# Kernel tuning notes

Hardware: AMD Instinct MI355X
Metric: run time of the kernel (lower is better)

## Reference

```python
import jax, jax.numpy as jnp
import numpy as np

N = 1_000_000   # detections
FDIM = 64       # embedding dim
C = 128         # number of clusters (track ids in [0, C))
DELTA_VAR = 0.5
DELTA_DIST = 3.0


def setup_inputs() -> dict:
    key = jax.random.key(0)
    k1, k2 = jax.random.split(key)
    features = jax.random.normal(k1, (N, FDIM), dtype=jnp.float32)
    labels = jax.random.randint(k2, (N, 2), 0, C, dtype=jnp.int32)  # [fr, track_id], all ids >= 0
    return {"features": features, "labels": labels}


def reference(features, labels):
    # All track ids are >= 0 by construction, so the tp_ids filter is a no-op
    # and the dynamic unique-cluster loop becomes a fixed-C segment reduce.
    ids = labels[:, 1]
    ones = jnp.ones((features.shape[0],), dtype=features.dtype)
    counts = jax.ops.segment_sum(ones, ids, num_segments=C)            # (C,)
    sums = jax.ops.segment_sum(features, ids, num_segments=C)         # (C, F)
    means = sums / counts[:, None]                                     # per-cluster mean

    # variance term: per-point distance to its cluster mean, hinged at delta_var
    d = jnp.linalg.norm(features - means[ids], axis=1)                 # (N,)
    per_pt = jnp.square(jax.nn.relu(d - DELTA_VAR))
    per_cluster = jax.ops.segment_sum(per_pt, ids, num_segments=C) / counts
    var_loss = jnp.sum(per_cluster) / C

    # pairwise cluster-distance term over i != j, hinged at delta_dist
    diff = means[:, None, :] - means[None, :, :]                       # (C, C, F)
    sq = jnp.sum(diff * diff, axis=-1)                                 # (C, C)
    eye = jnp.eye(C, dtype=bool)
    pd = jnp.sqrt(jnp.where(eye, 1.0, sq))                             # safe sqrt on diagonal
    dl = jnp.where(eye, 0.0, jnp.square(jax.nn.relu(DELTA_DIST - pd)))
    dist_loss = jnp.sum(dl) / (C * (C - 1))

    return var_loss + dist_loss
```

## Files before the change

kernel.cpp:

```cpp
#include <hip/hip_runtime.h>

#define NPTS 1000000
#define FDIM 64
#define CNUM 128
#define PSTRIDE 8320
#define NB1 1024
#define NB3 1024

typedef _Float16 half8 __attribute__((ext_vector_type(8)));
typedef float f32x4 __attribute__((ext_vector_type(4)));

__global__ __launch_bounds__(256, 4) void k1_partials(
    const float* __restrict__ feats, const int* __restrict__ labels,
    float* __restrict__ partials, int nblocks)
{
    __shared__ float lds[FDIM * 132];
    __shared__ float cnt[CNUM];
    const int tid = threadIdx.x;
    if (tid < CNUM) cnt[tid] = 0.f;
    __syncthreads();

    const int lane = tid & 63;
    const int n15 = lane & 15;
    const int kb = (lane >> 4) * 8;
    const int rowb = (lane >> 4) * 4;
    const int w = tid >> 6;
    const int fh = w & 1;
    const int fbase = fh * 32;
    const int nstreams = nblocks * 2;
    const int ts = ((blockIdx.x << 2) + w) >> 1;

    f32x4 acc[8][2];
    #pragma unroll
    for (int ct = 0; ct < 8; ++ct)
        #pragma unroll
        for (int nt = 0; nt < 2; ++nt)
            acc[ct][nt] = (f32x4){0.f, 0.f, 0.f, 0.f};

    const int ntiles = NPTS / 32;
    for (int t = ts; t < ntiles; t += nstreams) {
        const int p0 = t * 32;
        const float* fp = feats + (size_t)(p0 + kb) * FDIM + fbase + n15;
        const int* lp = labels + 2 * (p0 + kb) + 1;
        int vlab[8];
        #pragma unroll
        for (int i = 0; i < 8; ++i) vlab[i] = lp[2 * i];

        half8 B[2];
        #pragma unroll
        for (int nt = 0; nt < 2; ++nt) {
            #pragma unroll
            for (int i = 0; i < 8; ++i)
                B[nt][i] = (_Float16)fp[i * FDIM + nt * 16];
        }
        if (fh == 0 && lane < 32) {
            const int myl = labels[2 * (p0 + lane) + 1];
            atomicAdd(&cnt[myl], 1.0f);
        }
        #pragma unroll
        for (int ct = 0; ct < 8; ++ct) {
            const int cmine = ct * 16 + n15;
            union { unsigned u[4]; half8 h; } ua;
            #pragma unroll
            for (int j = 0; j < 4; ++j)
                ua.u[j] = ((vlab[2 * j] == cmine) ? 0x3C00u : 0u)
                        | ((vlab[2 * j + 1] == cmine) ? 0x3C000000u : 0u);
            #pragma unroll
            for (int nt = 0; nt < 2; ++nt)
                acc[ct][nt] = __builtin_amdgcn_mfma_f32_16x16x32_f16(
                    ua.h, B[nt], acc[ct][nt], 0, 0, 0);
        }
    }
    __syncthreads();

    for (int r = 0; r < 2; ++r) {
        if ((w >> 1) == r) {
            #pragma unroll
            for (int ct = 0; ct < 8; ++ct)
                #pragma unroll
                for (int nt = 0; nt < 2; ++nt) {
                    float* a = &lds[(fbase + nt * 16 + n15) * 132 + ct * 16 + rowb];
                    if (r == 0) *(f32x4*)a = acc[ct][nt];
                    else        *(f32x4*)a = *(f32x4*)a + acc[ct][nt];
                }
        }
        __syncthreads();
    }

    float* dst = partials + (size_t)blockIdx.x * PSTRIDE;
    for (int i4 = tid; i4 < 2048; i4 += 256) {
        const int f = i4 >> 5, c0 = (i4 & 31) * 4;
        ((float4*)dst)[i4] = *(float4*)&lds[f * 132 + c0];
    }
    if (tid < CNUM) dst[8192 + tid] = cnt[tid];
}

__global__ __launch_bounds__(256) void k2_reduce(
    const float* __restrict__ partials, int nblocks, float* __restrict__ red,
    float* __restrict__ ppsum, float* __restrict__ dsum, int* __restrict__ counter)
{
    const int tid = threadIdx.x;
    const int tsub = tid & 31, grp = tid >> 5;
    const int t0 = blockIdx.x * 32;
    float s = 0.f;
    #pragma unroll 8
    for (int b = grp; b < nblocks; b += 8)
        s += partials[(size_t)b * PSTRIDE + t0 + tsub];
    __shared__ float lred[8][33];
    lred[grp][tsub] = s;
    __syncthreads();
    if (tid < 32) {
        float tot = 0.f;
        #pragma unroll
        for (int q = 0; q < 8; ++q) tot += lred[q][tid];
        const int t = t0 + tid;
        if (t < 8192) red[(t & 127) * FDIM + (t >> 7)] = tot;
        else red[t] = tot;
    }
    if (blockIdx.x == 0) {
        if (tid >= 128) ppsum[tid - 128] = 0.f;
        if (tid == 64) dsum[0] = 0.f;
        if (tid == 65) counter[0] = 0;
    }
}

__global__ __launch_bounds__(256, 4) void k3_var(
    const float4* __restrict__ feats4, const int* __restrict__ labels,
    const float* __restrict__ red, float* __restrict__ ppsum, int nblocks)
{
    __shared__ float4 mu4[CNUM * 16];
    __shared__ float lpp[CNUM];
    const int tid = threadIdx.x;
    for (int i = tid; i < 2048; i += 256) {
        float4 sv = ((const float4*)red)[i];
        float ci = 1.0f / red[8192 + (i >> 4)];
        mu4[i] = make_float4(sv.x * ci, sv.y * ci, sv.z * ci, sv.w * ci);
    }
    if (tid < CNUM) lpp[tid] = 0.f;
    __syncthreads();

    const int lane = tid & 63;
    const int k = lane & 15, g = lane >> 4;
    const int nwaves = nblocks * 4;
    const int wid = ((blockIdx.x << 8) + tid) >> 6;
    const int ntiles = NPTS / 16;

    int b = wid;
    float4 v[4]; int cc = 0;
    if (b < ntiles) {
        const float4* fp = feats4 + (size_t)b * 256 + lane;
        #pragma unroll
        for (int s = 0; s < 4; ++s) v[s] = fp[s * 64];
        cc = labels[2 * (b * 16 + k) + 1];
    }
    while (b < ntiles) {
        const int bn = b + nwaves;
        float4 vn[4]; int ccn = 0;
        if (bn < ntiles) {
            const float4* fp = feats4 + (size_t)bn * 256 + lane;
            #pragma unroll
            for (int s = 0; s < 4; ++s) vn[s] = fp[s * 64];
            ccn = labels[2 * (bn * 16 + k) + 1];
        }
        #pragma unroll
        for (int s = 0; s < 4; ++s) {
            const int c = __shfl(cc, 4 * s + g);
            float4 m = mu4[c * 16 + k];
            float dx = v[s].x - m.x, dy = v[s].y - m.y,
                  dz = v[s].z - m.z, dw = v[s].w - m.w;
            float sq = dx * dx + dy * dy + dz * dz + dw * dw;
            sq += __shfl_xor(sq, 1); sq += __shfl_xor(sq, 2);
            sq += __shfl_xor(sq, 4); sq += __shfl_xor(sq, 8);
            if (k == 0) {
                const float t = sqrtf(sq) - 0.5f;
                if (t > 0.f) atomicAdd(&lpp[c], t * t);
            }
        }
        b = bn;
        #pragma unroll
        for (int s = 0; s < 4; ++s) v[s] = vn[s];
        cc = ccn;
    }
    __syncthreads();
    if (tid < CNUM) atomicAdd(&ppsum[tid], lpp[tid]);
}

__global__ __launch_bounds__(128) void k45_dist_final(
    const float* __restrict__ red, const float* __restrict__ ppsum,
    float* __restrict__ dsum, int* __restrict__ counter, float* __restrict__ out)
{
    __shared__ float4 mu4[CNUM * 17];
    __shared__ int lastflag;
    __shared__ float sv[2];
    const int tid = threadIdx.x;
    for (int i = tid; i < 2048; i += 128) {
        float4 s4 = ((const float4*)red)[i];
        float ci = 1.0f / red[8192 + (i >> 4)];
        mu4[(i >> 4) * 17 + (i & 15)] =
            make_float4(s4.x * ci, s4.y * ci, s4.z * ci, s4.w * ci);
    }
    __syncthreads();
    const int i = blockIdx.x, j = tid;
    float sq = 0.f;
    #pragma unroll
    for (int q = 0; q < 16; ++q) {
        float4 a = mu4[i * 17 + q], b = mu4[j * 17 + q];
        float dx = a.x - b.x, dy = a.y - b.y, dz = a.z - b.z, dw = a.w - b.w;
        sq += dx * dx + dy * dy + dz * dz + dw * dw;
    }
    float dl = 0.f;
    if (j != i) {
        const float r = 3.0f - sqrtf(sq);
        if (r > 0.f) dl = r * r;
    }
    #pragma unroll
    for (int m = 1; m < 64; m <<= 1) dl += __shfl_xor(dl, m);
    if ((tid & 63) == 0) atomicAdd(dsum, dl);
    __threadfence();
    __syncthreads();
    if (tid == 0) lastflag = (atomicAdd(counter, 1) == (int)gridDim.x - 1);
    __syncthreads();
    if (lastflag) {
        float v = ppsum[tid] / red[8192 + tid];
        #pragma unroll
        for (int m = 1; m < 64; m <<= 1) v += __shfl_xor(v, m);
        if ((tid & 63) == 0) sv[tid >> 6] = v;
    }
    __syncthreads();
    if (lastflag && tid == 0) {
        const float dtot = atomicAdd(dsum, 0.0f);
        out[0] = (sv[0] + sv[1]) / (float)CNUM
               + dtot / (float)(CNUM * (CNUM - 1));
    }
}

extern "C" void kernel_launch(void* const* d_in, const int* in_sizes, int n_in,
                              void* d_out, int out_size, void* d_ws, size_t ws_size,
                              hipStream_t stream) {
    (void)in_sizes; (void)n_in; (void)out_size;
    const float* feats   = (const float*)d_in[0];
    const float4* feats4 = (const float4*)d_in[0];
    const int* labels    = (const int*)d_in[1];
    float* ws            = (float*)d_ws;
    float* out           = (float*)d_out;

    int nb1 = NB1;
    {
        size_t avail = ws_size / sizeof(float);
        size_t fixed = PSTRIDE + 128 + 2;
        if (avail > fixed) {
            size_t cap = (avail - fixed) / PSTRIDE;
            if ((size_t)nb1 > cap) nb1 = (int)cap;
        } else nb1 = 1;
        if (nb1 < 1) nb1 = 1;
    }
    float* partials = ws;
    float* red      = ws + (size_t)nb1 * PSTRIDE;
    float* ppsum    = red + PSTRIDE;
    float* dsum     = ppsum + 128;
    int*   counter  = (int*)(dsum + 1);

    k1_partials<<<nb1, 256, 0, stream>>>(feats, labels, partials, nb1);
    k2_reduce<<<PSTRIDE / 32, 256, 0, stream>>>(partials, nb1, red, ppsum, dsum, counter);
    k3_var<<<NB3, 256, 0, stream>>>(feats4, labels, red, ppsum, NB3);
    k45_dist_final<<<CNUM, 128, 0, stream>>>(red, ppsum, dsum, counter, out);
}
```

Before: 132.9 us.

## Split k1 feature dims across four waves, prefetch next tile, drop LDS reduction

Each of the four waves in a k1 block now owns a distinct 16-feature slice of one shared 32-point tile, instead of pairs of waves handling 32 features on separate tile streams. The next tile's features and labels are register-prefetched while the current tile's MFMAs run. Accumulators are written straight to global memory in cluster-major order, which removes the LDS cross-wave reduction and the transposition in k2. The grid grows to 1280 blocks with an occupancy hint of 5, and k2 is reshaped to 16 columns by 16 block-groups, at the cost of more partial buffers to reduce and uncoalesced scattered stores from k1.

```diff
diff --git a/kernel.cpp b/kernel.cpp
--- a/kernel.cpp
+++ b/kernel.cpp
@@ -4,17 +4,16 @@
 #define FDIM 64
 #define CNUM 128
 #define PSTRIDE 8320
-#define NB1 1024
+#define NB1 1280
 #define NB3 1024
 
 typedef _Float16 half8 __attribute__((ext_vector_type(8)));
 typedef float f32x4 __attribute__((ext_vector_type(4)));
 
-__global__ __launch_bounds__(256, 4) void k1_partials(
+__global__ __launch_bounds__(256, 5) void k1_partials(
     const float* __restrict__ feats, const int* __restrict__ labels,
     float* __restrict__ partials, int nblocks)
 {
-    __shared__ float lds[FDIM * 132];
     __shared__ float cnt[CNUM];
     const int tid = threadIdx.x;
     if (tid < CNUM) cnt[tid] = 0.f;
@@ -24,74 +23,69 @@
     const int n15 = lane & 15;
     const int kb = (lane >> 4) * 8;
     const int rowb = (lane >> 4) * 4;
-    const int w = tid >> 6;
-    const int fh = w & 1;
-    const int fbase = fh * 32;
-    const int nstreams = nblocks * 2;
-    const int ts = ((blockIdx.x << 2) + w) >> 1;
-
-    f32x4 acc[8][2];
-    #pragma unroll
-    for (int ct = 0; ct < 8; ++ct)
-        #pragma unroll
-        for (int nt = 0; nt < 2; ++nt)
-            acc[ct][nt] = (f32x4){0.f, 0.f, 0.f, 0.f};
+    const int fq = tid >> 6;
+    const int fbase = fq * 16;
+
+    f32x4 acc[8];
+    #pragma unroll
+    for (int ct = 0; ct < 8; ++ct) acc[ct] = (f32x4){0.f, 0.f, 0.f, 0.f};
 
     const int ntiles = NPTS / 32;
-    for (int t = ts; t < ntiles; t += nstreams) {
+    int t = blockIdx.x;
+    float fv[8]; int vl[8]; int cl = 0;
+    if (t < ntiles) {
         const int p0 = t * 32;
         const float* fp = feats + (size_t)(p0 + kb) * FDIM + fbase + n15;
         const int* lp = labels + 2 * (p0 + kb) + 1;
-        int vlab[8];
-        #pragma unroll
-        for (int i = 0; i < 8; ++i) vlab[i] = lp[2 * i];
-
-        half8 B[2];
-        #pragma unroll
-        for (int nt = 0; nt < 2; ++nt) {
-            #pragma unroll
-            for (int i = 0; i < 8; ++i)
-                B[nt][i] = (_Float16)fp[i * FDIM + nt * 16];
-        }
-        if (fh == 0 && lane < 32) {
-            const int myl = labels[2 * (p0 + lane) + 1];
-            atomicAdd(&cnt[myl], 1.0f);
-        }
+        #pragma unroll
+        for (int i = 0; i < 8; ++i) fv[i] = fp[i * FDIM];
+        #pragma unroll
+        for (int i = 0; i < 8; ++i) vl[i] = lp[2 * i];
+        if (lane < 32) cl = labels[2 * (p0 + lane) + 1];
+    }
+    while (t < ntiles) {
+        const int tn = t + nblocks;
+        float fv2[8]; int vl2[8]; int cl2 = 0;
+        if (tn < ntiles) {
+            const int p0 = tn * 32;
+            const float* fp = feats + (size_t)(p0 + kb) * FDIM + fbase + n15;
+            const int* lp = labels + 2 * (p0 + kb) + 1;
+            #pragma unroll
+            for (int i = 0; i < 8; ++i) fv2[i] = fp[i * FDIM];
+            #pragma unroll
+            for (int i = 0; i < 8; ++i) vl2[i] = lp[2 * i];
+            if (lane < 32) cl2 = labels[2 * (p0 + lane) + 1];
+        }
+        if (fq == 0 && lane < 32) atomicAdd(&cnt[cl], 1.0f);
+
+        half8 B;
+        #pragma unroll
+        for (int i = 0; i < 8; ++i) B[i] = (_Float16)fv[i];
         #pragma unroll
         for (int ct = 0; ct < 8; ++ct) {
             const int cmine = ct * 16 + n15;
             union { unsigned u[4]; half8 h; } ua;
             #pragma unroll
             for (int j = 0; j < 4; ++j)
-                ua.u[j] = ((vlab[2 * j] == cmine) ? 0x3C00u : 0u)
-                        | ((vlab[2 * j + 1] == cmine) ? 0x3C000000u : 0u);
-            #pragma unroll
-            for (int nt = 0; nt < 2; ++nt)
-                acc[ct][nt] = __builtin_amdgcn_mfma_f32_16x16x32_f16(
-                    ua.h, B[nt], acc[ct][nt], 0, 0, 0);
-        }
-    }
-    __syncthreads();
-
-    for (int r = 0; r < 2; ++r) {
-        if ((w >> 1) == r) {
-            #pragma unroll
-            for (int ct = 0; ct < 8; ++ct)
-                #pragma unroll
-                for (int nt = 0; nt < 2; ++nt) {
-                    float* a = &lds[(fbase + nt * 16 + n15) * 132 + ct * 16 + rowb];
-                    if (r == 0) *(f32x4*)a = acc[ct][nt];
-                    else        *(f32x4*)a = *(f32x4*)a + acc[ct][nt];
-                }
-        }
-        __syncthreads();
-    }
+                ua.u[j] = ((vl[2 * j] == cmine) ? 0x3C00u : 0u)
+                        | ((vl[2 * j + 1] == cmine) ? 0x3C000000u : 0u);
+            acc[ct] = __builtin_amdgcn_mfma_f32_16x16x32_f16(ua.h, B, acc[ct], 0, 0, 0);
+        }
+        t = tn;
+        #pragma unroll
+        for (int i = 0; i < 8; ++i) { fv[i] = fv2[i]; vl[i] = vl2[i]; }
+        cl = cl2;
+    }
+    __syncthreads();
 
     float* dst = partials + (size_t)blockIdx.x * PSTRIDE;
-    for (int i4 = tid; i4 < 2048; i4 += 256) {
-        const int f = i4 >> 5, c0 = (i4 & 31) * 4;
-        ((float4*)dst)[i4] = *(float4*)&lds[f * 132 + c0];
-    }
+    #pragma unroll
+    for (int ct = 0; ct < 8; ++ct)
+        #pragma unroll
+        for (int reg = 0; reg < 4; ++reg) {
+            const int c = ct * 16 + rowb + reg;
+            dst[c * FDIM + fbase + n15] = acc[ct][reg];
+        }
     if (tid < CNUM) dst[8192 + tid] = cnt[tid];
 }
 
@@ -100,22 +94,20 @@
     float* __restrict__ ppsum, float* __restrict__ dsum, int* __restrict__ counter)
 {
     const int tid = threadIdx.x;
-    const int tsub = tid & 31, grp = tid >> 5;
-    const int t0 = blockIdx.x * 32;
+    const int tsub = tid & 15, grp = tid >> 4;
+    const int t0 = blockIdx.x * 16;
     float s = 0.f;
     #pragma unroll 8
-    for (int b = grp; b < nblocks; b += 8)
+    for (int b = grp; b < nblocks; b += 16)
         s += partials[(size_t)b * PSTRIDE + t0 + tsub];
-    __shared__ float lred[8][33];
+    __shared__ float lred[16][17];
     lred[grp][tsub] = s;
     __syncthreads();
-    if (tid < 32) {
+    if (tid < 16) {
         float tot = 0.f;
         #pragma unroll
-        for (int q = 0; q < 8; ++q) tot += lred[q][tid];
-        const int t = t0 + tid;
-        if (t < 8192) red[(t & 127) * FDIM + (t >> 7)] = tot;
-        else red[t] = tot;
+        for (int q = 0; q < 16; ++q) tot += lred[q][tid];
+        red[t0 + tid] = tot;
     }
     if (blockIdx.x == 0) {
         if (tid >= 128) ppsum[tid - 128] = 0.f;
@@ -261,7 +253,7 @@
     int*   counter  = (int*)(dsum + 1);
 
     k1_partials<<<nb1, 256, 0, stream>>>(feats, labels, partials, nb1);
-    k2_reduce<<<PSTRIDE / 32, 256, 0, stream>>>(partials, nb1, red, ppsum, dsum, counter);
+    k2_reduce<<<PSTRIDE / 16, 256, 0, stream>>>(partials, nb1, red, ppsum, dsum, counter);
     k3_var<<<NB3, 256, 0, stream>>>(feats4, labels, red, ppsum, NB3);
     k45_dist_final<<<CNUM, 128, 0, stream>>>(red, ppsum, dsum, counter, out);
 }
```

After: 149.6 us. +12.5%, slower.
